# Performance work log

Measured on AMD Instinct MI355X. Metric: run time of the kernel, lower is better.

The kernel has to match this reference:

```python
import jax, jax.numpy as jnp
import numpy as np
from jax import lax

# pywt db4 filters (8 taps)
_DEC_LO = np.array([-0.010597401784997278, 0.032883011666982945, 0.030841381835986965,
                    -0.18703481171888114, -0.02798376941698385, 0.6308807679295904,
                    0.7148465705525415, 0.23037781330885523])
_DEC_HI = np.array([-0.23037781330885523, 0.7148465705525415, -0.6308807679295904,
                    -0.02798376941698385, 0.18703481171888114, 0.030841381835986965,
                    -0.032883011666982945, -0.010597401784997278])
_REC_LO = _DEC_LO[::-1].copy()
_REC_HI = _DEC_HI[::-1].copy()
_L = 8  # filter length
LEVELS = 4


def _dwt_level(x):
    # x: (M, n) -> (cA, cD) each (M, (n+_L-1)//2), pywt 'symmetric' mode
    xe = jnp.pad(x, ((0, 0), (_L - 1, _L - 1)), mode='symmetric')[:, 1:]
    ker = jnp.stack([_DEC_LO[::-1], _DEC_HI[::-1]]).astype(x.dtype)[:, None, :]  # (2,1,L)
    y = lax.conv_general_dilated(xe[:, None, :], ker, (2,), 'VALID')  # (M,2,m)
    return y[:, 0], y[:, 1]


def _idwt_level(ca, cd, out_len):
    # inverse DWT, cropped to out_len (matches length of next-finer approximation)
    inp = jnp.stack([ca, cd], axis=1)  # (M,2,m)
    ker = jnp.stack([_REC_LO[::-1], _REC_HI[::-1]]).astype(ca.dtype)[None]  # (1,2,L)
    y = lax.conv_general_dilated(inp, ker, (1,), [(_L - 1, _L - 1)], lhs_dilation=(2,))
    return y[:, 0, _L - 2:_L - 2 + out_len]


def setup_inputs() -> dict:
    key = jax.random.key(0)
    k1, k2, k3, k4 = jax.random.split(key, 4)
    B, N, C = 32, 8192, 64
    m = N
    for _ in range(LEVELS):
        m = (m + _L - 1) // 2  # 518
    scale = 1.0 / (C * C)
    return {
        'x': jax.random.normal(k1, (B, N, C), jnp.float32),
        'w1': scale * jax.random.uniform(k2, (C, C, m), jnp.float32),
        'w2': scale * jax.random.uniform(k3, (C, C, m), jnp.float32),
        'dense_kernel': jax.random.normal(k4, (C, C), jnp.float32) / jnp.sqrt(C).astype(jnp.float32),
        'dense_bias': jnp.zeros((C,), jnp.float32),
    }


def reference(x, w1, w2, dense_kernel, dense_bias):
    B, N, C = x.shape
    xc = jnp.transpose(x, (0, 2, 1)).reshape(B * C, N)  # per-(batch,channel) signals
    # analysis: multi-level DWT
    lens, details = [], []
    a = xc
    for _ in range(LEVELS):
        lens.append(a.shape[1])
        a, d = _dwt_level(a)
        details.append(d)
    m = a.shape[1]
    # channel mixing on coarsest approximation and coarsest detail (WNO kernel)
    a = jnp.einsum('bim,iom->bom', a.reshape(B, C, m), w1).reshape(B * C, m)
    details[-1] = jnp.einsum('bim,iom->bom', details[-1].reshape(B, C, m), w2).reshape(B * C, m)
    # synthesis: multi-level IDWT
    for j in range(LEVELS - 1, -1, -1):
        a = _idwt_level(a, details[j], lens[j])
    y = jnp.transpose(a.reshape(B, C, N), (0, 2, 1))
    shortcut = x @ dense_kernel + dense_bias  # Dense 1x1 shortcut
    out = y + shortcut
    return out * jnp.tanh(jax.nn.softplus(out))  # mish
```

## Files before the change

### kernel.cpp

```cpp
#include <hip/hip_runtime.h>
#include <hip/hip_bf16.h>
#include <stdint.h>

typedef __attribute__((ext_vector_type(8))) short short8;
typedef __attribute__((ext_vector_type(4))) float floatx4;

__device__ __constant__ float c_DL[8] = {
    -0.010597401784997278f, 0.032883011666982945f, 0.030841381835986965f,
    -0.18703481171888114f, -0.02798376941698385f, 0.6308807679295904f,
    0.7148465705525415f, 0.23037781330885523f};
__device__ __constant__ float c_DH[8] = {
    -0.23037781330885523f, 0.7148465705525415f, -0.6308807679295904f,
    -0.02798376941698385f, 0.18703481171888114f, 0.030841381835986965f,
    -0.032883011666982945f, -0.010597401784997278f};
__device__ __constant__ float c_RL[8] = {
    0.23037781330885523f, 0.7148465705525415f, 0.6308807679295904f,
    -0.02798376941698385f, -0.18703481171888114f, 0.030841381835986965f,
    0.032883011666982945f, -0.010597401784997278f};
__device__ __constant__ float c_RH[8] = {
    -0.010597401784997278f, -0.032883011666982945f, 0.030841381835986965f,
    0.18703481171888114f, -0.02798376941698385f, -0.6308807679295904f,
    0.7148465705525415f, -0.23037781330885523f};

__device__ __forceinline__ float bflo(uint32_t u) { return __uint_as_float(u << 16); }
__device__ __forceinline__ float bfhi(uint32_t u) { return __uint_as_float(u & 0xffff0000u); }
__device__ __forceinline__ float ldf(const float* p, size_t i) { return p[i]; }
__device__ __forceinline__ float ldf(const __hip_bfloat16* p, size_t i) { return __bfloat162float(p[i]); }
__device__ __forceinline__ void stf(float* p, size_t i, float v) { p[i] = v; }
__device__ __forceinline__ void stf(__hip_bfloat16* p, size_t i, float v) { p[i] = __float2bfloat16(v); }
__device__ __forceinline__ short f2bs(float f) {
  __hip_bfloat16 h = __float2bfloat16(f);
  return *reinterpret_cast<short*>(&h);
}

__device__ __forceinline__ int reflect_idx(int t, int n) {
  if (t < 0) t = -1 - t;
  if (t >= n) t = 2 * n - 1 - t;
  return t;
}

#define S1R 4100
#define S2R 2056

#define NT1 134
__global__ __launch_bounds__(256) void k_dwt_first(const float* __restrict__ x,
                                                   __hip_bfloat16* __restrict__ outa,
                                                   __hip_bfloat16* __restrict__ outd) {
  const int b = blockIdx.y;
  const int k0 = blockIdx.x * 64;
  const int tid = threadIdx.x;
  __shared__ float xs[NT1 * 65];

  const float4* x4 = (const float4*)x;
  for (int idx = tid; idx < NT1 * 16; idx += 256) {
    int nl = idx >> 4, cq = idx & 15;
    int t = 2 * k0 - 6 + nl;
    int n = reflect_idx(t, 8192);
    float4 v = x4[((size_t)b * 8192 + n) * 16 + cq];
    float* d = &xs[nl * 65 + 4 * cq];
    d[0] = v.x; d[1] = v.y; d[2] = v.z; d[3] = v.w;
  }
  __syncthreads();

  const int kk = tid & 63;
  const int k = k0 + kk;
  if (k >= 4099) return;
  for (int c = (tid >> 6); c < 64; c += 4) {
    float lo = 0.f, hi = 0.f;
#pragma unroll
    for (int j = 0; j < 8; ++j) {
      float v = xs[(2 * kk + 7 - j) * 65 + c];
      lo += c_DL[j] * v;
      hi += c_DH[j] * v;
    }
    size_t s = (size_t)b * 64 + c;
    outa[s * S1R + k] = __float2bfloat16(lo);
    outd[s * S1R + k] = __float2bfloat16(hi);
  }
}

__global__ __launch_bounds__(256) void k_ana234(const __hip_bfloat16* __restrict__ a1,
                                                __hip_bfloat16* __restrict__ d2o,
                                                float* __restrict__ d3o,
                                                float* __restrict__ a4o,
                                                float* __restrict__ d4o) {
  const int r = blockIdx.x;
  const int tid = threadIdx.x;
  __shared__ float s1[4100];
  __shared__ float s2[2054];
  __shared__ float s3[1032];

  const uint2* row2 = (const uint2*)(a1 + (size_t)r * S1R);
  for (int i = tid; i < 1025; i += 256) {
    uint2 u = row2[i];
    int e = 4 * i;
    s1[e] = bflo(u.x); s1[e + 1] = bfhi(u.x);
    s1[e + 2] = bflo(u.y); s1[e + 3] = bfhi(u.y);
  }
  __syncthreads();

  for (int k = tid; k < 2053; k += 256) {
    float lo = 0.f, hi = 0.f;
    if (k >= 3 && k <= 2048) {
      const float2* p = (const float2*)&s1[2 * k - 6];
      float2 v0 = p[0], v1 = p[1], v2 = p[2], v3 = p[3];
      lo = c_RL[0]*v0.x + c_RL[1]*v0.y + c_RL[2]*v1.x + c_RL[3]*v1.y +
           c_RL[4]*v2.x + c_RL[5]*v2.y + c_RL[6]*v3.x + c_RL[7]*v3.y;
      hi = c_RH[0]*v0.x + c_RH[1]*v0.y + c_RH[2]*v1.x + c_RH[3]*v1.y +
           c_RH[4]*v2.x + c_RH[5]*v2.y + c_RH[6]*v3.x + c_RH[7]*v3.y;
    } else {
#pragma unroll
      for (int j = 0; j < 8; ++j) {
        float v = s1[reflect_idx(2 * k + 1 - j, 4099)];
        lo += c_DL[j] * v; hi += c_DH[j] * v;
      }
    }
    d2o[(size_t)r * S2R + k] = __float2bfloat16(hi);
    s2[k] = lo;
  }
  __syncthreads();

  for (int k = tid; k < 1030; k += 256) {
    float lo = 0.f, hi = 0.f;
    if (k >= 3 && k <= 1025) {
      const float2* p = (const float2*)&s2[2 * k - 6];
      float2 v0 = p[0], v1 = p[1], v2 = p[2], v3 = p[3];
      lo = c_RL[0]*v0.x + c_RL[1]*v0.y + c_RL[2]*v1.x + c_RL[3]*v1.y +
           c_RL[4]*v2.x + c_RL[5]*v2.y + c_RL[6]*v3.x + c_RL[7]*v3.y;
      hi = c_RH[0]*v0.x + c_RH[1]*v0.y + c_RH[2]*v1.x + c_RH[3]*v1.y +
           c_RH[4]*v2.x + c_RH[5]*v2.y + c_RH[6]*v3.x + c_RH[7]*v3.y;
    } else {
#pragma unroll
      for (int j = 0; j < 8; ++j) {
        float v = s2[reflect_idx(2 * k + 1 - j, 2053)];
        lo += c_DL[j] * v; hi += c_DH[j] * v;
      }
    }
    d3o[(size_t)r * 1030 + k] = hi;
    s3[k] = lo;
  }
  __syncthreads();

  for (int k = tid; k < 518; k += 256) {
    float lo = 0.f, hi = 0.f;
    if (k >= 3 && k <= 514) {
      const float2* p = (const float2*)&s3[2 * k - 6];
      float2 v0 = p[0], v1 = p[1], v2 = p[2], v3 = p[3];
      lo = c_RL[0]*v0.x + c_RL[1]*v0.y + c_RL[2]*v1.x + c_RL[3]*v1.y +
           c_RL[4]*v2.x + c_RL[5]*v2.y + c_RL[6]*v3.x + c_RL[7]*v3.y;
      hi = c_RH[0]*v0.x + c_RH[1]*v0.y + c_RH[2]*v1.x + c_RH[3]*v1.y +
           c_RH[4]*v2.x + c_RH[5]*v2.y + c_RH[6]*v3.x + c_RH[7]*v3.y;
    } else {
#pragma unroll
      for (int j = 0; j < 8; ++j) {
        float v = s3[reflect_idx(2 * k + 1 - j, 1030)];
        lo += c_DL[j] * v; hi += c_DH[j] * v;
      }
    }
    a4o[(size_t)r * 518 + k] = lo;
    d4o[(size_t)r * 518 + k] = hi;
  }
}

__global__ __launch_bounds__(256) void k_mix(const float* __restrict__ a4,
                                             const float* __restrict__ d4,
                                             const float* __restrict__ w1,
                                             const float* __restrict__ w2,
                                             float* __restrict__ am,
                                             float* __restrict__ dm) {
  int idx = blockIdx.y * 256 + threadIdx.x;
  if (idx >= 64 * 518) return;
  int o = idx / 518;
  int p = idx - o * 518;
  int b0 = blockIdx.x * 2;

  float a0 = 0.f, a1 = 0.f, dd0 = 0.f, dd1 = 0.f;

  const float* w1p = w1 + (size_t)o * 518 + p;
  const float* w2p = w2 + (size_t)o * 518 + p;
  const float* a4p = a4 + (size_t)b0 * 64 * 518 + p;
  const float* d4p = d4 + (size_t)b0 * 64 * 518 + p;

  for (int i = 0; i < 64; ++i) {
    float wa = w1p[(size_t)i * (64 * 518)];
    float wd = w2p[(size_t)i * (64 * 518)];
    size_t o0 = (size_t)i * 518;
    size_t o1 = (size_t)(64 + i) * 518;
    a0  += a4p[o0] * wa;
    a1  += a4p[o1] * wa;
    dd0 += d4p[o0] * wd;
    dd1 += d4p[o1] * wd;
  }
  size_t s0 = (size_t)(b0 * 64 + o) * 518 + p;
  size_t s1 = (size_t)((b0 + 1) * 64 + o) * 518 + p;
  am[s0] = a0;  am[s1] = a1;
  dm[s0] = dd0; dm[s1] = dd1;
}

__global__ __launch_bounds__(256) void k_syn32(const float* __restrict__ a4m,
                                               const float* __restrict__ d4m,
                                               const float* __restrict__ d3,
                                               __hip_bfloat16* __restrict__ r2out) {
  const int r = blockIdx.x;
  const int tid = threadIdx.x;
  __shared__ float sa[518], sd[518], s3d[1030], r3[1030];
  for (int i = tid; i < 518; i += 256) {
    sa[i] = a4m[(size_t)r * 518 + i];
    sd[i] = d4m[(size_t)r * 518 + i];
  }
  for (int i = tid; i < 1030; i += 256) s3d[i] = d3[(size_t)r * 1030 + i];
  __syncthreads();
  for (int s = tid; s < 1030; s += 256) {
    int u = s >> 1, par = s & 1;
    float acc = 0.f;
#pragma unroll
    for (int t = 0; t < 4; ++t) {
      int i = u + 3 - t;
      float fl = par ? c_RL[2 * t + 1] : c_RL[2 * t];
      float fh = par ? c_RH[2 * t + 1] : c_RH[2 * t];
      acc += fl * sa[i] + fh * sd[i];
    }
    r3[s] = acc;
  }
  __syncthreads();
  for (int s = tid; s < 2053; s += 256) {
    int u = s >> 1, par = s & 1;
    float acc = 0.f;
#pragma unroll
    for (int t = 0; t < 4; ++t) {
      int i = u + 3 - t;
      float fl = par ? c_RL[2 * t + 1] : c_RL[2 * t];
      float fh = par ? c_RH[2 * t + 1] : c_RH[2 * t];
      acc += fl * r3[i] + fh * s3d[i];
    }
    r2out[(size_t)r * S2R + s] = __float2bfloat16(acc);
  }
}

template <typename TCa, typename TCd, typename TOut>
__global__ void k_idwt(const TCa* __restrict__ ca, const TCd* __restrict__ cd,
                       TOut* __restrict__ out, int m, int out_len, int sin, int sout) {
  int s = blockIdx.x * blockDim.x + threadIdx.x;
  if (s >= out_len) return;
  const TCa* pa = ca + (size_t)blockIdx.y * sin;
  const TCd* pd = cd + (size_t)blockIdx.y * sin;
  int u = s >> 1, par = s & 1;
  float acc = 0.f;
#pragma unroll
  for (int t = 0; t < 4; ++t) {
    int i = u + 3 - t;
    float fl = par ? c_RL[2 * t + 1] : c_RL[2 * t];
    float fh = par ? c_RH[2 * t + 1] : c_RH[2 * t];
    acc += fl * ldf(pa, i) + fh * ldf(pd, i);
  }
  stf(out, (size_t)blockIdx.y * sout + s, acc);
}

__global__ __launch_bounds__(256) void k_epilogue(const __hip_bfloat16* __restrict__ r1,
                                                  const __hip_bfloat16* __restrict__ dd1,
                                                  const float* __restrict__ x,
                                                  const float* __restrict__ dk,
                                                  const float* __restrict__ bias,
                                                  float* __restrict__ out) {
  const int b = blockIdx.y;
  const int n0 = blockIdx.x * 64;
  const int u0 = n0 >> 1;
  const int tid = threadIdx.x;
  const int lane = tid & 63;
  const int w = tid >> 6;

  __shared__ __hip_bfloat16 Kt[64 * 72];
  __shared__ float ra[35 * 65];
  __shared__ float rd[35 * 65];

  {
    const float4* dk4 = (const float4*)dk;
    for (int idx = tid; idx < 1024; idx += 256) {
      int c = idx >> 4, o0 = (idx & 15) * 4;
      float4 v = dk4[idx];
      Kt[(o0 + 0) * 72 + c] = __float2bfloat16(v.x);
      Kt[(o0 + 1) * 72 + c] = __float2bfloat16(v.y);
      Kt[(o0 + 2) * 72 + c] = __float2bfloat16(v.z);
      Kt[(o0 + 3) * 72 + c] = __float2bfloat16(v.w);
    }
  }
  {
    int o2 = tid >> 2;
    const __hip_bfloat16* pr = r1 + (size_t)(b * 64 + o2) * S1R + u0;
    const __hip_bfloat16* pd = dd1 + (size_t)(b * 64 + o2) * S1R + u0;
    for (int il = (tid & 3); il < 35; il += 4) {
      ra[il * 65 + o2] = __bfloat162float(pr[il]);
      rd[il * 65 + o2] = __bfloat162float(pd[il]);
    }
  }
  __syncthreads();

  const int m16 = lane & 15;
  const int kq = (lane >> 4) * 8;
  const int nrow = w * 16 + m16;
  const float* xrow = x + ((size_t)b * 8192 + n0 + nrow) * 64;

  floatx4 acc[4];
#pragma unroll
  for (int ot = 0; ot < 4; ++ot) acc[ot] = (floatx4){0.f, 0.f, 0.f, 0.f};

#pragma unroll
  for (int ks = 0; ks < 2; ++ks) {
    float4 xa = *(const float4*)(xrow + ks * 32 + kq);
    float4 xb = *(const float4*)(xrow + ks * 32 + kq + 4);
    short8 af;
    af[0] = f2bs(xa.x); af[1] = f2bs(xa.y); af[2] = f2bs(xa.z); af[3] = f2bs(xa.w);
    af[4] = f2bs(xb.x); af[5] = f2bs(xb.y); af[6] = f2bs(xb.z); af[7] = f2bs(xb.w);
#pragma unroll
    for (int ot = 0; ot < 4; ++ot) {
      short8 bf = *(const short8*)&Kt[(ot * 16 + m16) * 72 + ks * 32 + kq];
      acc[ot] = __builtin_amdgcn_mfma_f32_16x16x32_bf16(af, bf, acc[ot], 0, 0, 0);
    }
  }

  const int rbase = (lane >> 4) * 4;
#pragma unroll
  for (int ot = 0; ot < 4; ++ot) {
    int o_loc = ot * 16 + m16;
    float bo = bias[o_loc];
#pragma unroll
    for (int rg = 0; rg < 4; ++rg) {
      int n_loc = w * 16 + rbase + rg;
      int ul = n_loc >> 1, par = n_loc & 1;
      float wv = 0.f;
#pragma unroll
      for (int t = 0; t < 4; ++t) {
        int i = ul + 3 - t;
        float fl = par ? c_RL[2 * t + 1] : c_RL[2 * t];
        float fh = par ? c_RH[2 * t + 1] : c_RH[2 * t];
        wv += fl * ra[i * 65 + o_loc] + fh * rd[i * 65 + o_loc];
      }
      float v = acc[ot][rg] + wv + bo;
      float e = __expf(fminf(v, 15.f));
      float num = e * (e + 2.f);
      float mm = (v > 15.f) ? v : v * (num / (num + 2.f));
      out[((size_t)b * 8192 + n0 + n_loc) * 64 + o_loc] = mm;
    }
  }
}

extern "C" void kernel_launch(void* const* d_in, const int* in_sizes, int n_in,
                              void* d_out, int out_size, void* d_ws, size_t ws_size,
                              hipStream_t stream) {
  const float* x    = (const float*)d_in[0];
  const float* w1   = (const float*)d_in[1];
  const float* w2   = (const float*)d_in[2];
  const float* dk   = (const float*)d_in[3];
  const float* bias = (const float*)d_in[4];
  float* out = (float*)d_out;

  const size_t R = 2048;

  float* wf = (float*)d_ws;
  float* d3f = wf; wf += R * 1030;
  float* a4f = wf; wf += R * 518;
  float* d4f = wf; wf += R * 518;
  float* a4m = wf; wf += R * 518;
  float* d4m = wf; wf += R * 518;
  __hip_bfloat16* wb = (__hip_bfloat16*)wf;
  __hip_bfloat16* a1b = wb; wb += R * S1R;
  __hip_bfloat16* d1b = wb; wb += R * S1R;
  __hip_bfloat16* a2b = wb; wb += R * S2R;
  __hip_bfloat16* d2b = wb; wb += R * S2R;

  k_dwt_first<<<dim3(65, 32), 256, 0, stream>>>(x, a1b, d1b);
  k_ana234<<<dim3(2048), 256, 0, stream>>>(a1b, d2b, d3f, a4f, d4f);
  k_mix<<<dim3(16, 130), 256, 0, stream>>>(a4f, d4f, w1, w2, a4m, d4m);
  k_syn32<<<dim3(2048), 256, 0, stream>>>(a4m, d4m, d3f, a2b);
  k_idwt<__hip_bfloat16, __hip_bfloat16, __hip_bfloat16>
      <<<dim3((4099 + 255) / 256, 2048), 256, 0, stream>>>(a2b, d2b, a1b, 2053, 4099, S2R, S1R);
  k_epilogue<<<dim3(128, 32), 256, 0, stream>>>(a1b, d1b, x, dk, bias, out);
}
```

Measured before the change: 300.7 us.

## Restructure channel-mix kernel to one block per mode with shared-memory reuse

Replaces the per-(o,p) mixing kernel, which re-read the weights once per batch pair across 16 blocks, with one block per mode p. Each block stages that mode's 64x64 w1/w2 slices and all 32 batches of a4/d4 into LDS, then computes a register-tiled 4-output by 2-batch outer product per thread. Weights are now read once in total instead of 16 times. Block indices are also remapped so that neighbouring p values land on the same XCD, to improve L2 locality for the strided gathers. The tradeoff is that the global loads are strided gathers (stride 518 floats), which coalesce poorly, and each block uses about 48KB of LDS.

```diff
diff --git a/kernel.cpp b/kernel.cpp
--- a/kernel.cpp
+++ b/kernel.cpp
@@ -162,39 +162,65 @@
   }
 }
 
-__global__ __launch_bounds__(256) void k_mix(const float* __restrict__ a4,
-                                             const float* __restrict__ d4,
-                                             const float* __restrict__ w1,
-                                             const float* __restrict__ w2,
-                                             float* __restrict__ am,
-                                             float* __restrict__ dm) {
-  int idx = blockIdx.y * 256 + threadIdx.x;
-  if (idx >= 64 * 518) return;
-  int o = idx / 518;
-  int p = idx - o * 518;
-  int b0 = blockIdx.x * 2;
-
-  float a0 = 0.f, a1 = 0.f, dd0 = 0.f, dd1 = 0.f;
-
-  const float* w1p = w1 + (size_t)o * 518 + p;
-  const float* w2p = w2 + (size_t)o * 518 + p;
-  const float* a4p = a4 + (size_t)b0 * 64 * 518 + p;
-  const float* d4p = d4 + (size_t)b0 * 64 * 518 + p;
-
+__global__ __launch_bounds__(256) void k_mix_p(const float* __restrict__ a4,
+                                               const float* __restrict__ d4,
+                                               const float* __restrict__ w1,
+                                               const float* __restrict__ w2,
+                                               float* __restrict__ am,
+                                               float* __restrict__ dm) {
+  const int bx = blockIdx.x;
+  const int xcd = bx & 7;
+  const int j = bx >> 3;
+  const int p = (xcd < 6) ? (xcd * 65 + j) : (390 + (xcd - 6) * 64 + j);
+
+  __shared__ float w1s[4096];
+  __shared__ float w2s[4096];
+  __shared__ float as[2048];
+  __shared__ float ds[2048];
+
+  const int tid = threadIdx.x;
+  for (int idx = tid; idx < 4096; idx += 256) {
+    w1s[idx] = w1[(size_t)idx * 518 + p];
+    w2s[idx] = w2[(size_t)idx * 518 + p];
+  }
+  for (int idx = tid; idx < 2048; idx += 256) {
+    int i = idx >> 5, b = idx & 31;
+    as[idx] = a4[(size_t)(b * 64 + i) * 518 + p];
+    ds[idx] = d4[(size_t)(b * 64 + i) * 518 + p];
+  }
+  __syncthreads();
+
+  const int o0 = (tid & 15) * 4;
+  const int bq = tid >> 4;
+  floatx4 acc0 = {0.f, 0.f, 0.f, 0.f}, acc1 = {0.f, 0.f, 0.f, 0.f};
+  floatx4 accd0 = {0.f, 0.f, 0.f, 0.f}, accd1 = {0.f, 0.f, 0.f, 0.f};
+
+#pragma unroll 4
   for (int i = 0; i < 64; ++i) {
-    float wa = w1p[(size_t)i * (64 * 518)];
-    float wd = w2p[(size_t)i * (64 * 518)];
-    size_t o0 = (size_t)i * 518;
-    size_t o1 = (size_t)(64 + i) * 518;
-    a0  += a4p[o0] * wa;
-    a1  += a4p[o1] * wa;
-    dd0 += d4p[o0] * wd;
-    dd1 += d4p[o1] * wd;
-  }
-  size_t s0 = (size_t)(b0 * 64 + o) * 518 + p;
-  size_t s1 = (size_t)((b0 + 1) * 64 + o) * 518 + p;
-  am[s0] = a0;  am[s1] = a1;
-  dm[s0] = dd0; dm[s1] = dd1;
+    floatx4 wv1 = *(const floatx4*)&w1s[i * 64 + o0];
+    floatx4 wv2 = *(const floatx4*)&w2s[i * 64 + o0];
+    float a0 = as[i * 32 + bq];
+    float a1 = as[i * 32 + bq + 16];
+    float dv0 = ds[i * 32 + bq];
+    float dv1 = ds[i * 32 + bq + 16];
+#pragma unroll
+    for (int q = 0; q < 4; ++q) {
+      acc0[q] += a0 * wv1[q];
+      acc1[q] += a1 * wv1[q];
+      accd0[q] += dv0 * wv2[q];
+      accd1[q] += dv1 * wv2[q];
+    }
+  }
+
+#pragma unroll
+  for (int q = 0; q < 4; ++q) {
+    size_t s0 = (size_t)(bq * 64 + o0 + q) * 518 + p;
+    size_t s1 = (size_t)((bq + 16) * 64 + o0 + q) * 518 + p;
+    am[s0] = acc0[q];
+    am[s1] = acc1[q];
+    dm[s0] = accd0[q];
+    dm[s1] = accd1[q];
+  }
 }
 
 __global__ __launch_bounds__(256) void k_syn32(const float* __restrict__ a4m,
@@ -370,7 +396,7 @@
 
   k_dwt_first<<<dim3(65, 32), 256, 0, stream>>>(x, a1b, d1b);
   k_ana234<<<dim3(2048), 256, 0, stream>>>(a1b, d2b, d3f, a4f, d4f);
-  k_mix<<<dim3(16, 130), 256, 0, stream>>>(a4f, d4f, w1, w2, a4m, d4m);
+  k_mix_p<<<dim3(518), 256, 0, stream>>>(a4f, d4f, w1, w2, a4m, d4m);
   k_syn32<<<dim3(2048), 256, 0, stream>>>(a4m, d4m, d3f, a2b);
   k_idwt<__hip_bfloat16, __hip_bfloat16, __hip_bfloat16>
       <<<dim3((4099 + 255) / 256, 2048), 256, 0, stream>>>(a2b, d2b, a1b, 2053, 4099, S2R, S1R);
```

Result: no change. 303.6 us (+1.0%).
